# Kernel tuning notes

Hardware: AMD Instinct MI355X
Metric: run time of the kernel (lower is better)

The kernel has to match this reference:

```python
import jax, jax.numpy as jnp
import numpy as np

S, B, D = 4096, 4, 1024
APERTURE = 256
SCALE = 1.0 / np.sqrt(D)
EPS = 1e-6
NEG_INF = -jnp.inf


def _xavier(key, shape, gain=np.sqrt(2.0)):
    fan_in, fan_out = shape[1], shape[0]
    a = gain * np.sqrt(6.0 / (fan_in + fan_out))
    return jax.random.uniform(key, shape, jnp.float32, -a, a)


def setup_inputs() -> dict:
    key = jax.random.key(0)
    ks = jax.random.split(key, 8)
    return {
        "x": jax.random.normal(ks[0], (S, B, D), jnp.float32),
        "Wk": _xavier(ks[1], (D, D)),
        "Wq": _xavier(ks[2], (D, D)),
        "Wv": _xavier(ks[3], (D, D)),
        "Wp": _xavier(ks[4], (D, D)),
        "W1": _xavier(ks[5], (D, D)),
        "b1": jnp.full((D,), 0.1, jnp.float32),
        "W2": _xavier(ks[6], (1, D)),
        "b2": jnp.full((1,), 0.1, jnp.float32),
        "gamma": jnp.ones((D,), jnp.float32),
        "beta": jnp.zeros((D,), jnp.float32),
    }


def _layer_norm(y, gamma, beta):
    m = jnp.mean(y, axis=-1, keepdims=True)
    v = jnp.mean((y - m) ** 2, axis=-1, keepdims=True)
    return (y - m) * jax.lax.rsqrt(v + EPS) * gamma + beta


def reference(x, Wk, Wq, Wv, Wp, W1, b1, W2, b2, gamma, beta):
    # x: (S, B, D) -> (B, S, D)
    xb = jnp.transpose(x, (1, 0, 2))
    K = jnp.einsum('bsd,ed->bse', xb, Wk)
    Q = jnp.einsum('bsd,ed->bse', xb, Wq)
    V = jnp.einsum('bsd,ed->bse', xb, Wv)
    e = jnp.einsum('bqd,bkd->bqk', Q, K) * SCALE  # (B, S, S)
    # ignore_self: -inf on diagonal
    eye = jnp.eye(S, dtype=bool)
    e = jnp.where(eye[None, :, :], NEG_INF, e)
    # aperture mask: torch masks where tril(e,ap)*triu(e,-ap) == 0
    scope = jnp.tril(e, APERTURE) * jnp.triu(e, -APERTURE)
    e = jnp.where(scope == 0, NEG_INF, e)
    alpha = jax.nn.softmax(e, axis=2)  # dropout is identity at eval
    c = jnp.einsum('bqk,bkd->bqd', alpha, V)
    c = jnp.einsum('bqd,ed->bqe', c, Wp)
    y = c + xb
    y = _layer_norm(y, gamma, beta)
    y = jax.nn.relu(jnp.einsum('bsd,ed->bse', y, W1) + b1)
    y = _layer_norm(y, gamma, beta)
    y = jax.nn.sigmoid(jnp.einsum('bsd,ed->bse', y, W2) + b2)  # (B, S, 1)
    return jnp.transpose(y, (1, 0, 2))  # (S, B, 1)
```

## Files before the change

### kernel.cpp

```cpp
#include <hip/hip_runtime.h>
#include <stdint.h>
#include <math.h>

#define S_LEN 4096
#define BATCH 4
#define DIM   1024
#define AP    256
#define BANDC 768
#define SCALE 0.03125f

typedef __attribute__((ext_vector_type(4))) float f32x4;
typedef __attribute__((ext_vector_type(8))) short bf16x8;

__device__ __forceinline__ ushort f2bf(float f) {
  union { float f; uint32_t u; } v; v.f = f;
  uint32_t r = v.u + 0x7FFFu + ((v.u >> 16) & 1u);
  return (ushort)(r >> 16);
}
__device__ __forceinline__ float bf2f(ushort u) {
  union { uint32_t u; float f; } v; v.u = ((uint32_t)u) << 16; return v.f;
}
__device__ __forceinline__ ushort f2h(float f) {
  union { _Float16 h; ushort u; } v; v.h = (_Float16)f; return v.u;
}
__device__ __forceinline__ float h2f(ushort u) {
  union { ushort u; _Float16 h; } v; v.u = u; return (float)v.h;
}

__device__ __forceinline__ void gload16(const void* g, void* l) {
  __builtin_amdgcn_global_load_lds((const __attribute__((address_space(1))) void*)g,
                                   (__attribute__((address_space(3))) void*)l,
                                   16, 0, 0);
}

__device__ __forceinline__ float wave_sum(float v) {
  #pragma unroll
  for (int o = 32; o > 0; o >>= 1) v += __shfl_xor(v, o, 64);
  return v;
}
__device__ __forceinline__ float wave_max(float v) {
  #pragma unroll
  for (int o = 32; o > 0; o >>= 1) v = fmaxf(v, __shfl_xor(v, o, 64));
  return v;
}

#define STAGE2(dstbase, g0, g1, kcol) \
  gload16((g0) + (kcol), lds + (dstbase) + stOff); \
  gload16((g1) + (kcol), lds + (dstbase) + 4096 + stOff);

#define MFMA16(arow, av, bv) \
  __builtin_amdgcn_s_setprio(1); \
  _Pragma("unroll") for (int m = 0; m < 4; ++m) \
  _Pragma("unroll") for (int n = 0; n < 4; ++n) \
    acc[(arow) + m][n] = __builtin_amdgcn_mfma_f32_16x16x32_bf16(av[m], bv[n], acc[(arow) + m][n], 0, 0, 0); \
  __builtin_amdgcn_s_setprio(0);

#define PHASE_CUT() \
  __builtin_amdgcn_sched_barrier(0); \
  asm volatile("s_barrier" ::: "memory");

__device__ __forceinline__ void gemm256_core(
    const ushort* __restrict__ Ablk, int lda,
    const ushort* __restrict__ Bblk, int ldb,
    int K, ushort* __restrict__ lds,
    f32x4 acc[8][4])
{
  const int tid  = threadIdx.x;
  const int lane = tid & 63;
  const int wave = tid >> 6;
  const int wr = wave >> 2;
  const int wn = wave & 3;

  const int srow = tid >> 2;
  const int gseg = (tid & 3) ^ ((tid >> 3) & 3);
  const ushort* gA0 = Ablk + (size_t)srow * lda + gseg * 8;
  const ushort* gA1 = Ablk + (size_t)(srow + 128) * lda + gseg * 8;
  const ushort* gB0 = Bblk + (size_t)srow * ldb + gseg * 8;
  const ushort* gB1 = Bblk + (size_t)(srow + 128) * ldb + gseg * 8;
  const int stOff = wave * 512;

  const int l15 = lane & 15;
  const int seg = (lane >> 4) ^ ((lane >> 1) & 3);
  const int raBase = (wr * 128 + l15) * 32 + seg * 8;
  const int rbBase = (wn * 64  + l15) * 32 + seg * 8;

  const int NT = K >> 6;

  STAGE2(0,     gA0, gA1, 0)
  STAGE2(16384, gB0, gB1, 0)
  STAGE2(8192,  gA0, gA1, 32)
  STAGE2(24576, gB0, gB1, 32)
  asm volatile("s_waitcnt vmcnt(4)" ::: "memory");
  asm volatile("s_barrier" ::: "memory");

  bf16x8 aE[4], aO[4], bE[4], bO[4];
  #pragma unroll
  for (int m = 0; m < 4; ++m) aE[m] = *(const bf16x8*)(lds + raBase + m * 512);
  #pragma unroll
  for (int n = 0; n < 4; ++n) bE[n] = *(const bf16x8*)(lds + 16384 + rbBase + n * 512);

  for (int t = 0; t < NT; ++t) {
    const int rb = (t & 1) * 32768;
    const int sb = rb ^ 32768;
    const int k1 = (t + 1) << 6;
    const bool more = (t + 1 < NT);

    #pragma unroll
    for (int m = 0; m < 4; ++m) aO[m] = *(const bf16x8*)(lds + rb + raBase + (m + 4) * 512);
    if (more) {
      STAGE2(sb,         gA0, gA1, k1)
      STAGE2(sb + 16384, gB0, gB1, k1)
    }
    MFMA16(0, aE, bE)
    if (more) asm volatile("s_waitcnt vmcnt(4)" ::: "memory");
    else      asm volatile("s_waitcnt vmcnt(0)" ::: "memory");
    PHASE_CUT()

    #pragma unroll
    for (int m = 0; m < 4; ++m) aE[m] = *(const bf16x8*)(lds + rb + 8192 + raBase + m * 512);
    #pragma unroll
    for (int n = 0; n < 4; ++n) bO[n] = *(const bf16x8*)(lds + rb + 24576 + rbBase + n * 512);
    if (more) {
      STAGE2(sb + 8192,  gA0, gA1, k1 + 32)
      STAGE2(sb + 24576, gB0, gB1, k1 + 32)
    }
    MFMA16(4, aO, bE)
    PHASE_CUT()

    #pragma unroll
    for (int m = 0; m < 4; ++m) aO[m] = *(const bf16x8*)(lds + rb + 8192 + raBase + (m + 4) * 512);
    MFMA16(0, aE, bO)
    if (more) asm volatile("s_waitcnt vmcnt(4)" ::: "memory");
    PHASE_CUT()

    if (more) {
      #pragma unroll
      for (int m = 0; m < 4; ++m) aE[m] = *(const bf16x8*)(lds + sb + raBase + m * 512);
      #pragma unroll
      for (int n = 0; n < 4; ++n) bE[n] = *(const bf16x8*)(lds + sb + 16384 + rbBase + n * 512);
    }
    MFMA16(4, aO, bO)
    PHASE_CUT()
  }
}

#define ACC256_ZERO(acc) \
  _Pragma("unroll") for (int m_ = 0; m_ < 8; m_++) \
  _Pragma("unroll") for (int n_ = 0; n_ < 4; n_++) \
  _Pragma("unroll") for (int r_ = 0; r_ < 4; r_++) acc[m_][n_][r_] = 0.0f;

__device__ __forceinline__ void epi256_store_bf16(
    f32x4 acc[8][4], ushort* __restrict__ lds,
    ushort* __restrict__ dst, int rowbase, int colb)
{
  __syncthreads();
  const int lane_ = threadIdx.x & 63;
  const int wave_ = threadIdx.x >> 6;
  const int wrb_ = (wave_ >> 2) * 128;
  const int wnb_ = (wave_ & 3) * 64;
  const int rb_ = (lane_ >> 4) << 2;
  const int cb_ = lane_ & 15;
  #pragma unroll
  for (int m = 0; m < 8; m++)
    #pragma unroll
    for (int n = 0; n < 4; n++)
      #pragma unroll
      for (int r = 0; r < 4; r++) {
        const int rl = wrb_ + m * 16 + rb_ + r;
        const int cl = wnb_ + n * 16 + cb_;
        const int cs = cl ^ (((rl >> 2) & 3) << 4);
        lds[rl * 256 + cs] = f2bf(acc[m][n][r]);
      }
  __syncthreads();
  #pragma unroll
  for (int it = 0; it < 16; ++it) {
    const int chunk = it * 512 + threadIdx.x;
    const int rl = chunk >> 5;
    const int c16 = chunk & 31;
    const int csw = (c16 * 16) ^ (((rl >> 2) & 3) << 5);
    bf16x8 v = *(const bf16x8*)((const char*)lds + rl * 512 + csw);
    *(bf16x8*)(dst + (size_t)(rowbase + rl) * DIM + colb + c16 * 8) = v;
  }
}

__device__ __forceinline__ void epi256_store_relu_bf16(
    f32x4 acc[8][4], ushort* __restrict__ lds,
    ushort* __restrict__ dst, int rowbase, int colb,
    const float* __restrict__ bias)
{
  __syncthreads();
  const int lane_ = threadIdx.x & 63;
  const int wave_ = threadIdx.x >> 6;
  const int wrb_ = (wave_ >> 2) * 128;
  const int wnb_ = (wave_ & 3) * 64;
  const int rb_ = (lane_ >> 4) << 2;
  const int cb_ = lane_ & 15;
  #pragma unroll
  for (int m = 0; m < 8; m++)
    #pragma unroll
    for (int n = 0; n < 4; n++) {
      const int cl = wnb_ + n * 16 + cb_;
      const float bv = bias[colb + cl];
      #pragma unroll
      for (int r = 0; r < 4; r++) {
        const int rl = wrb_ + m * 16 + rb_ + r;
        const int cs = cl ^ (((rl >> 2) & 3) << 4);
        lds[rl * 256 + cs] = f2bf(fmaxf(acc[m][n][r] + bv, 0.0f));
      }
    }
  __syncthreads();
  #pragma unroll
  for (int it = 0; it < 16; ++it) {
    const int chunk = it * 512 + threadIdx.x;
    const int rl = chunk >> 5;
    const int c16 = chunk & 31;
    const int csw = (c16 * 16) ^ (((rl >> 2) & 3) << 5);
    bf16x8 v = *(const bf16x8*)((const char*)lds + rl * 512 + csw);
    *(bf16x8*)(dst + (size_t)(rowbase + rl) * DIM + colb + c16 * 8) = v;
  }
}

#define EPI256_BEGIN(acc) { \
  const int lane_ = threadIdx.x & 63; \
  const int wave_ = threadIdx.x >> 6; \
  const int wrb_ = (wave_ >> 2) * 128; \
  const int wnb_ = (wave_ & 3) * 64; \
  const int rb_ = (lane_ >> 4) << 2; \
  const int cb_ = lane_ & 15; \
  _Pragma("unroll") for (int m_ = 0; m_ < 8; m_++) \
  _Pragma("unroll") for (int n_ = 0; n_ < 4; n_++) \
  _Pragma("unroll") for (int r_ = 0; r_ < 4; r_++) { \
    const int rloc = wrb_ + m_ * 16 + rb_ + r_; \
    const int cloc = wnb_ + n_ * 16 + cb_; \
    const float aval = acc[m_][n_][r_];
#define EPI256_END() } }

__global__ __launch_bounds__(256) void prep_x(const float* __restrict__ x, ushort* __restrict__ xb) {
  size_t idx = ((size_t)blockIdx.x * 256 + threadIdx.x) * 4;
  int d = (int)(idx & 1023);
  int s = (int)((idx >> 10) & 4095);
  int b = (int)(idx >> 22);
  float4 v = *(const float4*)(x + ((size_t)s * BATCH + b) * DIM + d);
  ushort4 o;
  o.x = f2bf(v.x); o.y = f2bf(v.y); o.z = f2bf(v.z); o.w = f2bf(v.w);
  *(ushort4*)(xb + idx) = o;
}

__global__ __launch_bounds__(256) void f2bf_all(
    const float* __restrict__ Wk, const float* __restrict__ Wq, const float* __restrict__ Wv,
    const float* __restrict__ Wp, const float* __restrict__ W1,
    ushort* __restrict__ wqkv, ushort* __restrict__ wpb, ushort* __restrict__ w1b)
{
  const int g = blockIdx.x;
  const int which = g >> 10;
  const int idx = ((g & 1023) * 256 + threadIdx.x) * 4;
  const float* src = (which == 0) ? Wk : (which == 1) ? Wq : (which == 2) ? Wv
                   : (which == 3) ? Wp : W1;
  ushort* dst = (which == 0) ? wqkv : (which == 1) ? wqkv + 1048576
              : (which == 2) ? wqkv + 2097152 : (which == 3) ? wpb : w1b;
  float4 v = *(const float4*)(src + idx);
  ushort4 o;
  o.x = f2bf(v.x); o.y = f2bf(v.y); o.z = f2bf(v.z); o.w = f2bf(v.w);
  *(ushort4*)(dst + idx) = o;
}

__global__ __launch_bounds__(512, 2) void qkv_gemm256(
    const ushort* __restrict__ xb, const ushort* __restrict__ wqkv,
    ushort* __restrict__ Kp, ushort* __restrict__ Qp, ushort* __restrict__ Vp)
{
  __shared__ ushort lds[65536];
  const int nid = (blockIdx.x & 7) * 96 + (blockIdx.x >> 3);
  const int by = nid / 12;
  const int bx = nid % 12;
  f32x4 acc[8][4];
  ACC256_ZERO(acc)
  gemm256_core(xb + (size_t)by * 256 * DIM, DIM,
               wqkv + (size_t)bx * 256 * DIM, DIM, DIM, lds, acc);
  ushort* dst = (bx < 4) ? Kp : (bx < 8) ? Qp : Vp;
  epi256_store_bf16(acc, lds, dst, by * 256, (bx & 3) * 256);
}

__global__ __launch_bounds__(512, 2) void scores_gemm256(
    const ushort* __restrict__ Qp, const ushort* __restrict__ Kp,
    ushort* __restrict__ eb)
{
  const int bid = blockIdx.x;
  const int b   = bid / 48;
  const int rem = bid % 48;
  const int i   = rem / 3;
  const int jj  = rem % 3;
  const int jblk = i + jj - 1;
  if (jblk < 0 || jblk >= 16) return;
  __shared__ ushort lds[65536];
  f32x4 acc[8][4];
  ACC256_ZERO(acc)
  gemm256_core(Qp + ((size_t)b * S_LEN + i * 256) * DIM, DIM,
               Kp + ((size_t)b * S_LEN + jblk * 256) * DIM, DIM, DIM, lds, acc);
  EPI256_BEGIN(acc)
    int q = i * 256 + rloc;
    int k = jblk * 256 + cloc;
    float v = aval * SCALE;
    int d = q - k;
    if (d == 0 || d > AP || d < -AP) v = -INFINITY;
    eb[((size_t)(b * S_LEN + q)) * BANDC + jj * 256 + cloc] = f2h(v);
  EPI256_END()
}

__global__ __launch_bounds__(512, 2) void av_gemm256(
    const ushort* __restrict__ aband, const ushort* __restrict__ VT,
    ushort* __restrict__ cbuf)
{
  __shared__ ushort lds[65536];
  const int bid  = blockIdx.x;
  const int b    = bid >> 6;
  const int i    = (bid >> 2) & 15;
  const int dblk = bid & 3;
  const int klo = (i == 0) ? 256 : 0;
  const int khi = (i == 15) ? 512 : BANDC;
  f32x4 acc[8][4];
  ACC256_ZERO(acc)
  const ushort* Ablk = aband + ((size_t)(b * S_LEN + i * 256)) * BANDC + klo;
  const ushort* Bblk = VT + (size_t)b * DIM * S_LEN + (size_t)dblk * 256 * S_LEN
                     + ((i - 1) * 256 + klo);
  gemm256_core(Ablk, BANDC, Bblk, S_LEN, khi - klo, lds, acc);
  epi256_store_bf16(acc, lds, cbuf, b * S_LEN + i * 256, dblk * 256);
}

__global__ __launch_bounds__(512, 2) void wp_gemm256(
    const ushort* __restrict__ cbuf, const ushort* __restrict__ wpb,
    const float* __restrict__ x, float* __restrict__ y0)
{
  __shared__ ushort lds[65536];
  const int nid = (blockIdx.x & 7) * 32 + (blockIdx.x >> 3);
  const int by = nid >> 2;
  const int bx = nid & 3;
  f32x4 acc[8][4];
  ACC256_ZERO(acc)
  gemm256_core(cbuf + (size_t)by * 256 * DIM, DIM,
               wpb + (size_t)bx * 256 * DIM, DIM, DIM, lds, acc);
  EPI256_BEGIN(acc)
    int row = by * 256 + rloc;
    int col = bx * 256 + cloc;
    int b = row >> 12, s = row & 4095;
    y0[(size_t)row * DIM + col] = aval + x[((size_t)s * BATCH + b) * DIM + col];
  EPI256_END()
}

__global__ __launch_bounds__(512, 2) void ffn1_gemm256(
    const ushort* __restrict__ y1, const ushort* __restrict__ w1b,
    const float* __restrict__ b1, ushort* __restrict__ h0)
{
  __shared__ ushort lds[65536];
  const int nid = (blockIdx.x & 7) * 32 + (blockIdx.x >> 3);
  const int by = nid >> 2;
  const int bx = nid & 3;
  f32x4 acc[8][4];
  ACC256_ZERO(acc)
  gemm256_core(y1 + (size_t)by * 256 * DIM, DIM,
               w1b + (size_t)bx * 256 * DIM, DIM, DIM, lds, acc);
  epi256_store_relu_bf16(acc, lds, h0, by * 256, bx * 256, b1);
}

__global__ __launch_bounds__(256) void transpose_v(const ushort* __restrict__ V, ushort* __restrict__ VT) {
  __shared__ ushort tile[64][66];
  const int s0 = blockIdx.x * 64, d0 = blockIdx.y * 64, b = blockIdx.z;
  const ushort* Vb = V + (size_t)b * S_LEN * DIM;
  ushort* VTb = VT + (size_t)b * DIM * S_LEN;
  #pragma unroll
  for (int it = 0; it < 16; it++) {
    int flat = it * 256 + threadIdx.x;
    int r = flat >> 6, c = flat & 63;
    tile[r][c] = Vb[(size_t)(s0 + r) * DIM + d0 + c];
  }
  __syncthreads();
  #pragma unroll
  for (int it = 0; it < 16; it++) {
    int flat = it * 256 + threadIdx.x;
    int r = flat >> 6, c = flat & 63;
    VTb[(size_t)(d0 + r) * S_LEN + s0 + c] = tile[c][r];
  }
}

__global__ __launch_bounds__(256) void softmax768(const ushort* __restrict__ eb,
                                                  ushort* __restrict__ aband)
{
  const int row  = blockIdx.x * 4 + (threadIdx.x >> 6);
  const int lane = threadIdx.x & 63;
  const int s    = row & 4095;
  const int i256 = s >> 8;
  const ushort* e = eb + (size_t)row * BANDC;
  ushort* ab = aband + (size_t)row * BANDC;

  float vals[12];
  bool  ok[12];
  float mx = -INFINITY;
  #pragma unroll
  for (int j = 0; j < 6; ++j) {
    const int c0 = (j * 64 + lane) * 2;
    ushort2 u = *(const ushort2*)(e + c0);
    #pragma unroll
    for (int t = 0; t < 2; ++t) {
      const int c = c0 + t;
      const int jblk = i256 + (c >> 8) - 1;
      const int k = jblk * 256 + (c & 255);
      const int d = s - k;
      const bool valid = (jblk >= 0) && (jblk < 16) && (d != 0) && (d <= AP) && (d >= -AP);
      ok[j * 2 + t] = valid;
      float v = valid ? h2f(t ? u.y : u.x) : -INFINITY;
      vals[j * 2 + t] = v;
      mx = fmaxf(mx, v);
    }
  }
  mx = wave_max(mx);
  float ss = 0.0f;
  #pragma unroll
  for (int t = 0; t < 12; ++t) {
    float ev = ok[t] ? __expf(vals[t] - mx) : 0.0f;
    vals[t] = ev;
    ss += ev;
  }
  float inv = 1.0f / wave_sum(ss);
  #pragma unroll
  for (int j = 0; j < 6; ++j) {
    const int c0 = (j * 64 + lane) * 2;
    ushort2 o;
    o.x = f2bf(vals[j * 2 + 0] * inv);
    o.y = f2bf(vals[j * 2 + 1] * inv);
    *(ushort2*)(ab + c0) = o;
  }
}

__global__ __launch_bounds__(256) void ln4(const float* __restrict__ y0, ushort* __restrict__ y1,
                                           const float* __restrict__ gamma, const float* __restrict__ beta)
{
  const int row  = blockIdx.x * 4 + (threadIdx.x >> 6);
  const int lane = threadIdx.x & 63;
  const float* r = y0 + (size_t)row * DIM;
  float4 v[4];
  float sum = 0.0f;
  #pragma unroll
  for (int j = 0; j < 4; ++j) {
    v[j] = *(const float4*)(r + j * 256 + lane * 4);
    sum += v[j].x + v[j].y + v[j].z + v[j].w;
  }
  const float mean = wave_sum(sum) * (1.0f / DIM);
  float q2 = 0.0f;
  #pragma unroll
  for (int j = 0; j < 4; ++j) {
    float a = v[j].x - mean, bq = v[j].y - mean, c = v[j].z - mean, d = v[j].w - mean;
    q2 += a * a + bq * bq + c * c + d * d;
  }
  const float rstd = rsqrtf(wave_sum(q2) * (1.0f / DIM) + 1e-6f);
  #pragma unroll
  for (int j = 0; j < 4; ++j) {
    const int d0 = j * 256 + lane * 4;
    float4 g = *(const float4*)(gamma + d0);
    float4 bb = *(const float4*)(beta + d0);
    ushort4 o;
    o.x = f2bf((v[j].x - mean) * rstd * g.x + bb.x);
    o.y = f2bf((v[j].y - mean) * rstd * g.y + bb.y);
    o.z = f2bf((v[j].z - mean) * rstd * g.z + bb.z);
    o.w = f2bf((v[j].w - mean) * rstd * g.w + bb.w);
    *(ushort4*)(y1 + (size_t)row * DIM + d0) = o;
  }
}

__global__ __launch_bounds__(256) void head4(const ushort* __restrict__ h0,
    const float* __restrict__ gamma, const float* __restrict__ beta,
    const float* __restrict__ W2, const float* __restrict__ b2,
    float* __restrict__ out)
{
  const int row  = blockIdx.x * 4 + (threadIdx.x >> 6);
  const int lane = threadIdx.x & 63;
  const int b = row >> 12, s = row & 4095;
  const ushort* r = h0 + (size_t)row * DIM;
  float v[16];
  float sum = 0.0f;
  #pragma unroll
  for (int j = 0; j < 4; ++j) {
    ushort4 u = *(const ushort4*)(r + j * 256 + lane * 4);
    v[j * 4 + 0] = bf2f(u.x); v[j * 4 + 1] = bf2f(u.y);
    v[j * 4 + 2] = bf2f(u.z); v[j * 4 + 3] = bf2f(u.w);
    sum += v[j * 4] + v[j * 4 + 1] + v[j * 4 + 2] + v[j * 4 + 3];
  }
  const float mean = wave_sum(sum) * (1.0f / DIM);
  float q2 = 0.0f;
  #pragma unroll
  for (int t = 0; t < 16; ++t) { float d = v[t] - mean; q2 += d * d; }
  const float rstd = rsqrtf(wave_sum(q2) * (1.0f / DIM) + 1e-6f);
  float part = 0.0f;
  #pragma unroll
  for (int j = 0; j < 4; ++j) {
    const int d0 = j * 256 + lane * 4;
    float4 g = *(const float4*)(gamma + d0);
    float4 bb = *(const float4*)(beta + d0);
    float4 w2 = *(const float4*)(W2 + d0);
    part += ((v[j * 4 + 0] - mean) * rstd * g.x + bb.x) * w2.x
          + ((v[j * 4 + 1] - mean) * rstd * g.y + bb.y) * w2.y
          + ((v[j * 4 + 2] - mean) * rstd * g.z + bb.z) * w2.z
          + ((v[j * 4 + 3] - mean) * rstd * g.w + bb.w) * w2.w;
  }
  const float logit = wave_sum(part) + b2[0];
  if (lane == 0) out[(size_t)s * BATCH + b] = 1.0f / (1.0f + expf(-logit));
}

extern "C" void kernel_launch(void* const* d_in, const int* in_sizes, int n_in,
                              void* d_out, int out_size, void* d_ws, size_t ws_size,
                              hipStream_t stream) {
  const float* x     = (const float*)d_in[0];
  const float* Wk    = (const float*)d_in[1];
  const float* Wq    = (const float*)d_in[2];
  const float* Wv    = (const float*)d_in[3];
  const float* Wp    = (const float*)d_in[4];
  const float* W1    = (const float*)d_in[5];
  const float* b1    = (const float*)d_in[6];
  const float* W2    = (const float*)d_in[7];
  const float* b2    = (const float*)d_in[8];
  const float* gamma = (const float*)d_in[9];
  const float* beta  = (const float*)d_in[10];
  float* out = (float*)d_out;

  char* w = (char*)d_ws;
  ushort* xb   = (ushort*)(w + 0);
  ushort* wqkv = (ushort*)(w + 33554432);
  ushort* wpb  = (ushort*)(w + 39845888);
  ushort* w1b  = (ushort*)(w + 41943040);
  ushort* Qp   = (ushort*)(w + 44040192);
  ushort* Kp   = (ushort*)(w + 77594624);
  ushort* Vp   = (ushort*)(w + 111149056);
  ushort* VT   = (ushort*)(w + 144703488);
  float*  big  = (float*)(w + 178257920);
  ushort* eband = (ushort*)big;
  ushort* aband = Qp;
  ushort* cbuf  = Kp;
  ushort* y1    = Vp;
  ushort* h0    = xb;
  float* y0     = big;

  prep_x<<<16384, 256, 0, stream>>>(x, xb);
  f2bf_all<<<5120, 256, 0, stream>>>(Wk, Wq, Wv, Wp, W1, wqkv, wpb, w1b);

  qkv_gemm256<<<768, 512, 0, stream>>>(xb, wqkv, Kp, Qp, Vp);
  transpose_v<<<dim3(64, 16, 4), 256, 0, stream>>>(Vp, VT);
  scores_gemm256<<<192, 512, 0, stream>>>(Qp, Kp, eband);
  softmax768<<<4096, 256, 0, stream>>>(eband, aband);
  av_gemm256<<<256, 512, 0, stream>>>(aband, VT, cbuf);
  wp_gemm256<<<256, 512, 0, stream>>>(cbuf, wpb, x, y0);
  ln4<<<4096, 256, 0, stream>>>(y0, y1, gamma, beta);
  ffn1_gemm256<<<256, 512, 0, stream>>>(y1, w1b, b1, h0);
  head4<<<4096, 256, 0, stream>>>(h0, gamma, beta, W2, b2, out);
}
```

Baseline: 363.4 us.

## Fuse V transpose into QKV epilogue, store residual in bf16, merge prep kernels

The QKV GEMM epilogue now writes V directly in transposed layout through an LDS transpose, so the separate transpose_v kernel and its extra read and write of V are gone. The Wp GEMM epilogue adds the residual and stores y0 as bf16 instead of fp32, halving the traffic into the LayerNorm kernel, which now reads with 16-byte vectors. The x and weight conversion kernels are merged into one launch, and the head kernel uses wider loads. Rounding the pre-LayerNorm activation to bf16 adds some precision loss.

```diff
diff --git a/kernel.cpp b/kernel.cpp
--- a/kernel.cpp
+++ b/kernel.cpp
@@ -170,6 +170,78 @@
         const int cl = wnb_ + n * 16 + cb_;
         const int cs = cl ^ (((rl >> 2) & 3) << 4);
         lds[rl * 256 + cs] = f2bf(acc[m][n][r]);
+      }
+  __syncthreads();
+  #pragma unroll
+  for (int it = 0; it < 16; ++it) {
+    const int chunk = it * 512 + threadIdx.x;
+    const int rl = chunk >> 5;
+    const int c16 = chunk & 31;
+    const int csw = (c16 * 16) ^ (((rl >> 2) & 3) << 5);
+    bf16x8 v = *(const bf16x8*)((const char*)lds + rl * 512 + csw);
+    *(bf16x8*)(dst + (size_t)(rowbase + rl) * DIM + colb + c16 * 8) = v;
+  }
+}
+
+__device__ __forceinline__ void epi256_store_vt(
+    f32x4 acc[8][4], ushort* __restrict__ lds,
+    ushort* __restrict__ VTb, int dbase, int sbase)
+{
+  __syncthreads();
+  const int lane_ = threadIdx.x & 63;
+  const int wave_ = threadIdx.x >> 6;
+  const int wrb_ = (wave_ >> 2) * 128;
+  const int wnb_ = (wave_ & 3) * 64;
+  const int rb_ = (lane_ >> 4) << 2;
+  const int cb_ = lane_ & 15;
+  #pragma unroll
+  for (int m = 0; m < 8; m++)
+    #pragma unroll
+    for (int n = 0; n < 4; n++)
+      #pragma unroll
+      for (int r = 0; r < 4; r++) {
+        const int rl = wrb_ + m * 16 + rb_ + r;
+        const int cl = wnb_ + n * 16 + cb_;
+        const int inner = rl ^ (((cl >> 2) & 3) << 4);
+        lds[cl * 256 + inner] = f2bf(acc[m][n][r]);
+      }
+  __syncthreads();
+  #pragma unroll
+  for (int it = 0; it < 16; ++it) {
+    const int chunk = it * 512 + threadIdx.x;
+    const int R = chunk >> 5;
+    const int c16 = chunk & 31;
+    const int csw = (c16 * 16) ^ (((R >> 2) & 3) << 5);
+    bf16x8 v = *(const bf16x8*)((const char*)lds + R * 512 + csw);
+    *(bf16x8*)(VTb + (size_t)(dbase + R) * S_LEN + sbase + c16 * 8) = v;
+  }
+}
+
+__device__ __forceinline__ void epi256_store_res_bf16(
+    f32x4 acc[8][4], ushort* __restrict__ lds,
+    ushort* __restrict__ dst, int rowbase, int colb,
+    const float* __restrict__ x)
+{
+  __syncthreads();
+  const int lane_ = threadIdx.x & 63;
+  const int wave_ = threadIdx.x >> 6;
+  const int wrb_ = (wave_ >> 2) * 128;
+  const int wnb_ = (wave_ & 3) * 64;
+  const int rb_ = (lane_ >> 4) << 2;
+  const int cb_ = lane_ & 15;
+  #pragma unroll
+  for (int m = 0; m < 8; m++)
+    #pragma unroll
+    for (int n = 0; n < 4; n++)
+      #pragma unroll
+      for (int r = 0; r < 4; r++) {
+        const int rl = wrb_ + m * 16 + rb_ + r;
+        const int cl = wnb_ + n * 16 + cb_;
+        const int row = rowbase + rl;
+        const int s = row & 4095, b = row >> 12;
+        const float xv = x[((size_t)s * BATCH + b) * DIM + colb + cl];
+        const int cs = cl ^ (((rl >> 2) & 3) << 4);
+        lds[rl * 256 + cs] = f2bf(acc[m][n][r] + xv);
       }
   __syncthreads();
   #pragma unroll
@@ -235,38 +307,41 @@
     const float aval = acc[m_][n_][r_];
 #define EPI256_END() } }
 
-__global__ __launch_bounds__(256) void prep_x(const float* __restrict__ x, ushort* __restrict__ xb) {
-  size_t idx = ((size_t)blockIdx.x * 256 + threadIdx.x) * 4;
-  int d = (int)(idx & 1023);
-  int s = (int)((idx >> 10) & 4095);
-  int b = (int)(idx >> 22);
-  float4 v = *(const float4*)(x + ((size_t)s * BATCH + b) * DIM + d);
-  ushort4 o;
-  o.x = f2bf(v.x); o.y = f2bf(v.y); o.z = f2bf(v.z); o.w = f2bf(v.w);
-  *(ushort4*)(xb + idx) = o;
-}
-
-__global__ __launch_bounds__(256) void f2bf_all(
+__global__ __launch_bounds__(256) void prep_all(
+    const float* __restrict__ x,
     const float* __restrict__ Wk, const float* __restrict__ Wq, const float* __restrict__ Wv,
     const float* __restrict__ Wp, const float* __restrict__ W1,
-    ushort* __restrict__ wqkv, ushort* __restrict__ wpb, ushort* __restrict__ w1b)
+    ushort* __restrict__ xb, ushort* __restrict__ wqkv,
+    ushort* __restrict__ wpb, ushort* __restrict__ w1b)
 {
   const int g = blockIdx.x;
-  const int which = g >> 10;
-  const int idx = ((g & 1023) * 256 + threadIdx.x) * 4;
-  const float* src = (which == 0) ? Wk : (which == 1) ? Wq : (which == 2) ? Wv
-                   : (which == 3) ? Wp : W1;
-  ushort* dst = (which == 0) ? wqkv : (which == 1) ? wqkv + 1048576
-              : (which == 2) ? wqkv + 2097152 : (which == 3) ? wpb : w1b;
-  float4 v = *(const float4*)(src + idx);
-  ushort4 o;
-  o.x = f2bf(v.x); o.y = f2bf(v.y); o.z = f2bf(v.z); o.w = f2bf(v.w);
-  *(ushort4*)(dst + idx) = o;
+  if (g < 16384) {
+    size_t idx = ((size_t)g * 256 + threadIdx.x) * 4;
+    int d = (int)(idx & 1023);
+    int s = (int)((idx >> 10) & 4095);
+    int b = (int)(idx >> 22);
+    float4 v = *(const float4*)(x + ((size_t)s * BATCH + b) * DIM + d);
+    ushort4 o;
+    o.x = f2bf(v.x); o.y = f2bf(v.y); o.z = f2bf(v.z); o.w = f2bf(v.w);
+    *(ushort4*)(xb + idx) = o;
+  } else {
+    const int gg = g - 16384;
+    const int which = gg >> 10;
+    const int idx = ((gg & 1023) * 256 + threadIdx.x) * 4;
+    const float* src = (which == 0) ? Wk : (which == 1) ? Wq : (which == 2) ? Wv
+                     : (which == 3) ? Wp : W1;
+    ushort* dst = (which == 0) ? wqkv : (which == 1) ? wqkv + 1048576
+                : (which == 2) ? wqkv + 2097152 : (which == 3) ? wpb : w1b;
+    float4 v = *(const float4*)(src + idx);
+    ushort4 o;
+    o.x = f2bf(v.x); o.y = f2bf(v.y); o.z = f2bf(v.z); o.w = f2bf(v.w);
+    *(ushort4*)(dst + idx) = o;
+  }
 }
 
 __global__ __launch_bounds__(512, 2) void qkv_gemm256(
     const ushort* __restrict__ xb, const ushort* __restrict__ wqkv,
-    ushort* __restrict__ Kp, ushort* __restrict__ Qp, ushort* __restrict__ Vp)
+    ushort* __restrict__ Kp, ushort* __restrict__ Qp, ushort* __restrict__ VT)
 {
   __shared__ ushort lds[65536];
   const int nid = (blockIdx.x & 7) * 96 + (blockIdx.x >> 3);
@@ -276,8 +351,13 @@
   ACC256_ZERO(acc)
   gemm256_core(xb + (size_t)by * 256 * DIM, DIM,
                wqkv + (size_t)bx * 256 * DIM, DIM, DIM, lds, acc);
-  ushort* dst = (bx < 4) ? Kp : (bx < 8) ? Qp : Vp;
-  epi256_store_bf16(acc, lds, dst, by * 256, (bx & 3) * 256);
+  if (bx < 8) {
+    ushort* dst = (bx < 4) ? Kp : Qp;
+    epi256_store_bf16(acc, lds, dst, by * 256, (bx & 3) * 256);
+  } else {
+    const int b = by >> 4, s0 = (by & 15) * 256;
+    epi256_store_vt(acc, lds, VT + (size_t)b * DIM * S_LEN, (bx & 3) * 256, s0);
+  }
 }
 
 __global__ __launch_bounds__(512, 2) void scores_gemm256(
@@ -328,7 +408,7 @@
 
 __global__ __launch_bounds__(512, 2) void wp_gemm256(
     const ushort* __restrict__ cbuf, const ushort* __restrict__ wpb,
-    const float* __restrict__ x, float* __restrict__ y0)
+    const float* __restrict__ x, ushort* __restrict__ y0)
 {
   __shared__ ushort lds[65536];
   const int nid = (blockIdx.x & 7) * 32 + (blockIdx.x >> 3);
@@ -338,12 +418,7 @@
   ACC256_ZERO(acc)
   gemm256_core(cbuf + (size_t)by * 256 * DIM, DIM,
                wpb + (size_t)bx * 256 * DIM, DIM, DIM, lds, acc);
-  EPI256_BEGIN(acc)
-    int row = by * 256 + rloc;
-    int col = bx * 256 + cloc;
-    int b = row >> 12, s = row & 4095;
-    y0[(size_t)row * DIM + col] = aval + x[((size_t)s * BATCH + b) * DIM + col];
-  EPI256_END()
+  epi256_store_res_bf16(acc, lds, y0, by * 256, bx * 256, x);
 }
 
 __global__ __launch_bounds__(512, 2) void ffn1_gemm256(
@@ -359,26 +434,6 @@
   gemm256_core(y1 + (size_t)by * 256 * DIM, DIM,
                w1b + (size_t)bx * 256 * DIM, DIM, DIM, lds, acc);
   epi256_store_relu_bf16(acc, lds, h0, by * 256, bx * 256, b1);
-}
-
-__global__ __launch_bounds__(256) void transpose_v(const ushort* __restrict__ V, ushort* __restrict__ VT) {
-  __shared__ ushort tile[64][66];
-  const int s0 = blockIdx.x * 64, d0 = blockIdx.y * 64, b = blockIdx.z;
-  const ushort* Vb = V + (size_t)b * S_LEN * DIM;
-  ushort* VTb = VT + (size_t)b * DIM * S_LEN;
-  #pragma unroll
-  for (int it = 0; it < 16; it++) {
-    int flat = it * 256 + threadIdx.x;
-    int r = flat >> 6, c = flat & 63;
-    tile[r][c] = Vb[(size_t)(s0 + r) * DIM + d0 + c];
-  }
-  __syncthreads();
-  #pragma unroll
-  for (int it = 0; it < 16; it++) {
-    int flat = it * 256 + threadIdx.x;
-    int r = flat >> 6, c = flat & 63;
-    VTb[(size_t)(d0 + r) * S_LEN + s0 + c] = tile[c][r];
-  }
 }
 
 __global__ __launch_bounds__(256) void softmax768(const ushort* __restrict__ eb,
@@ -430,38 +485,39 @@
   }
 }
 
-__global__ __launch_bounds__(256) void ln4(const float* __restrict__ y0, ushort* __restrict__ y1,
+__global__ __launch_bounds__(256) void ln4(const ushort* __restrict__ y0, ushort* __restrict__ y1,
                                            const float* __restrict__ gamma, const float* __restrict__ beta)
 {
   const int row  = blockIdx.x * 4 + (threadIdx.x >> 6);
   const int lane = threadIdx.x & 63;
-  const float* r = y0 + (size_t)row * DIM;
-  float4 v[4];
+  const ushort* r = y0 + (size_t)row * DIM;
+  float v[16];
   float sum = 0.0f;
   #pragma unroll
-  for (int j = 0; j < 4; ++j) {
-    v[j] = *(const float4*)(r + j * 256 + lane * 4);
-    sum += v[j].x + v[j].y + v[j].z + v[j].w;
+  for (int j = 0; j < 2; ++j) {
+    bf16x8 u = *(const bf16x8*)(r + j * 512 + lane * 8);
+    #pragma unroll
+    for (int t = 0; t < 8; ++t) { float f = bf2f((ushort)u[t]); v[j * 8 + t] = f; sum += f; }
   }
   const float mean = wave_sum(sum) * (1.0f / DIM);
   float q2 = 0.0f;
   #pragma unroll
-  for (int j = 0; j < 4; ++j) {
-    float a = v[j].x - mean, bq = v[j].y - mean, c = v[j].z - mean, d = v[j].w - mean;
-    q2 += a * a + bq * bq + c * c + d * d;
-  }
+  for (int t = 0; t < 16; ++t) { float d = v[t] - mean; q2 += d * d; }
   const float rstd = rsqrtf(wave_sum(q2) * (1.0f / DIM) + 1e-6f);
   #pragma unroll
-  for (int j = 0; j < 4; ++j) {
-    const int d0 = j * 256 + lane * 4;
-    float4 g = *(const float4*)(gamma + d0);
-    float4 bb = *(const float4*)(beta + d0);
-    ushort4 o;
-    o.x = f2bf((v[j].x - mean) * rstd * g.x + bb.x);
-    o.y = f2bf((v[j].y - mean) * rstd * g.y + bb.y);
-    o.z = f2bf((v[j].z - mean) * rstd * g.z + bb.z);
-    o.w = f2bf((v[j].w - mean) * rstd * g.w + bb.w);
-    *(ushort4*)(y1 + (size_t)row * DIM + d0) = o;
+  for (int j = 0; j < 2; ++j) {
+    const int d0 = j * 512 + lane * 8;
+    bf16x8 o;
+    #pragma unroll
+    for (int t = 0; t < 8; t += 4) {
+      float4 g = *(const float4*)(gamma + d0 + t);
+      float4 bb = *(const float4*)(beta + d0 + t);
+      o[t + 0] = (short)f2bf((v[j * 8 + t + 0] - mean) * rstd * g.x + bb.x);
+      o[t + 1] = (short)f2bf((v[j * 8 + t + 1] - mean) * rstd * g.y + bb.y);
+      o[t + 2] = (short)f2bf((v[j * 8 + t + 2] - mean) * rstd * g.z + bb.z);
+      o[t + 3] = (short)f2bf((v[j * 8 + t + 3] - mean) * rstd * g.w + bb.w);
+    }
+    *(bf16x8*)(y1 + (size_t)row * DIM + d0) = o;
   }
 }
 
@@ -477,11 +533,10 @@
   float v[16];
   float sum = 0.0f;
   #pragma unroll
-  for (int j = 0; j < 4; ++j) {
-    ushort4 u = *(const ushort4*)(r + j * 256 + lane * 4);
-    v[j * 4 + 0] = bf2f(u.x); v[j * 4 + 1] = bf2f(u.y);
-    v[j * 4 + 2] = bf2f(u.z); v[j * 4 + 3] = bf2f(u.w);
-    sum += v[j * 4] + v[j * 4 + 1] + v[j * 4 + 2] + v[j * 4 + 3];
+  for (int j = 0; j < 2; ++j) {
+    bf16x8 u = *(const bf16x8*)(r + j * 512 + lane * 8);
+    #pragma unroll
+    for (int t = 0; t < 8; ++t) { float f = bf2f((ushort)u[t]); v[j * 8 + t] = f; sum += f; }
   }
   const float mean = wave_sum(sum) * (1.0f / DIM);
   float q2 = 0.0f;
@@ -490,15 +545,18 @@
   const float rstd = rsqrtf(wave_sum(q2) * (1.0f / DIM) + 1e-6f);
   float part = 0.0f;
   #pragma unroll
-  for (int j = 0; j < 4; ++j) {
-    const int d0 = j * 256 + lane * 4;
-    float4 g = *(const float4*)(gamma + d0);
-    float4 bb = *(const float4*)(beta + d0);
-    float4 w2 = *(const float4*)(W2 + d0);
-    part += ((v[j * 4 + 0] - mean) * rstd * g.x + bb.x) * w2.x
-          + ((v[j * 4 + 1] - mean) * rstd * g.y + bb.y) * w2.y
-          + ((v[j * 4 + 2] - mean) * rstd * g.z + bb.z) * w2.z
-          + ((v[j * 4 + 3] - mean) * rstd * g.w + bb.w) * w2.w;
+  for (int j = 0; j < 2; ++j) {
+    const int d0 = j * 512 + lane * 8;
+    #pragma unroll
+    for (int t = 0; t < 8; t += 4) {
+      float4 g = *(const float4*)(gamma + d0 + t);
+      float4 bb = *(const float4*)(beta + d0 + t);
+      float4 w2 = *(const float4*)(W2 + d0 + t);
+      part += ((v[j * 8 + t + 0] - mean) * rstd * g.x + bb.x) * w2.x
+            + ((v[j * 8 + t + 1] - mean) * rstd * g.y + bb.y) * w2.y
+            + ((v[j * 8 + t + 2] - mean) * rstd * g.z + bb.z) * w2.z
+            + ((v[j * 8 + t + 3] - mean) * rstd * g.w + bb.w) * w2.w;
+    }
   }
   const float logit = wave_sum(part) + b2[0];
   if (lane == 0) out[(size_t)s * BATCH + b] = 1.0f / (1.0f + expf(-logit));
@@ -527,21 +585,18 @@
   ushort* w1b  = (ushort*)(w + 41943040);
   ushort* Qp   = (ushort*)(w + 44040192);
   ushort* Kp   = (ushort*)(w + 77594624);
-  ushort* Vp   = (ushort*)(w + 111149056);
+  ushort* y1   = (ushort*)(w + 111149056);
   ushort* VT   = (ushort*)(w + 144703488);
-  float*  big  = (float*)(w + 178257920);
+  char*   big  = (w + 178257920);
   ushort* eband = (ushort*)big;
   ushort* aband = Qp;
   ushort* cbuf  = Kp;
-  ushort* y1    = Vp;
   ushort* h0    = xb;
-  float* y0     = big;
-
-  prep_x<<<16384, 256, 0, stream>>>(x, xb);
-  f2bf_all<<<5120, 256, 0, stream>>>(Wk, Wq, Wv, Wp, W1, wqkv, wpb, w1b);
-
-  qkv_gemm256<<<768, 512, 0, stream>>>(xb, wqkv, Kp, Qp, Vp);
-  transpose_v<<<dim3(64, 16, 4), 256, 0, stream>>>(Vp, VT);
+  ushort* y0    = (ushort*)big;
+
+  prep_all<<<21504, 256, 0, stream>>>(x, Wk, Wq, Wv, Wp, W1, xb, wqkv, wpb, w1b);
+
+  qkv_gemm256<<<768, 512, 0, stream>>>(xb, wqkv, Kp, Qp, VT);
   scores_gemm256<<<192, 512, 0, stream>>>(Qp, Kp, eband);
   softmax768<<<4096, 256, 0, stream>>>(eband, aband);
   av_gemm256<<<256, 512, 0, stream>>>(aband, VT, cbuf);
```

New measurement: 335.8 us (median of 2 runs). 7.6% less time.
